# Optimization experiments

Measured on AMD Instinct MI355X. Metric: run time of the kernel, lower is better.

The kernel has to match this reference:

```python
import jax, jax.numpy as jnp
import numpy as np
import math

NUM_GROUPS = 32
NUM_HEADS = 8
EPS = 1e-5

def group_norm(x, w, b):
    B, C, H, W = x.shape
    xg = x.reshape(B, NUM_GROUPS, C // NUM_GROUPS, H, W)
    mu = xg.mean(axis=(2, 3, 4), keepdims=True)
    var = xg.var(axis=(2, 3, 4), keepdims=True)
    xn = ((xg - mu) * jax.lax.rsqrt(var + EPS)).reshape(B, C, H, W)
    return xn * w[None, :, None, None] + b[None, :, None, None]

def layer_norm(t, w, b):
    mu = t.mean(axis=-1, keepdims=True)
    var = t.var(axis=-1, keepdims=True)
    return (t - mu) * jax.lax.rsqrt(var + EPS) * w + b

def setup_inputs() -> dict:
    key = jax.random.key(0)
    ks = jax.random.split(key, 6)
    B, C, H, W, L, D = 32, 512, 32, 32, 77, 768
    return {
        "x": jax.random.normal(ks[0], (B, C, H, W), dtype=jnp.float32),
        "t": jax.random.normal(ks[1], (B, L, D), dtype=jnp.float32),
        "gn_w": jnp.ones((C,), jnp.float32),
        "gn_b": jnp.zeros((C,), jnp.float32),
        "ln_w": jnp.ones((D,), jnp.float32),
        "ln_b": jnp.zeros((D,), jnp.float32),
        "Wq": jax.random.normal(ks[2], (C, C), dtype=jnp.float32) * (1.0 / math.sqrt(C)),
        "Wkv": jax.random.normal(ks[3], (2 * C, D), dtype=jnp.float32) * (1.0 / math.sqrt(D)),
        "Wp": jax.random.normal(ks[4], (C, C), dtype=jnp.float32) * (1.0 / math.sqrt(C)),
        "bp": jnp.zeros((C,), jnp.float32),
    }

def reference(x, t, gn_w, gn_b, ln_w, ln_b, Wq, Wkv, Wp, bp):
    B, C, H, W = x.shape
    L = t.shape[1]
    hd = C // NUM_HEADS
    # q = 1x1 conv (no bias) on GroupNorm(x): [B,C,H,W]
    q = jnp.einsum('bchw,oc->bohw', group_norm(x, gn_w, gn_b), Wq)
    q = q.reshape(B, NUM_HEADS, hd, H * W)            # [B,h,hd,HW]
    # kv = Linear (no bias) on LayerNorm(t): [B,L,2C] -> [B,L,h,2*hd]
    kv = jnp.einsum('bld,od->blo', layer_norm(t, ln_w, ln_b), Wkv)
    kv = kv.reshape(B, L, NUM_HEADS, 2 * hd).transpose(0, 2, 3, 1)  # [B,h,2*hd,L]
    k, v = kv[:, :, :hd, :], kv[:, :, hd:, :]
    scale = 1.0 / math.sqrt(math.sqrt(hd))
    attn = jnp.einsum('bhct,bhcs->bhts', q * scale, k * scale)  # [B,h,HW,L]
    attn = jax.nn.softmax(attn, axis=-1)
    h = jnp.einsum('bhts,bhcs->bhct', attn, v).reshape(B, C, H, W)
    out = jnp.einsum('bchw,oc->bohw', h, Wp) + bp[None, :, None, None]
    return out + x
```

## Files before the change

### kernel.cpp

```cpp
#include <hip/hip_runtime.h>
#include <math.h>

#define NBATCH 32
#define NCH    512
#define NHW    1024
#define NL     77
#define ND     768
#define NHEADS 8

typedef __attribute__((ext_vector_type(8)))  short bf16x8;
typedef __attribute__((ext_vector_type(4)))  float f32x4;
typedef __attribute__((ext_vector_type(4)))  unsigned short ushort4v;
typedef __attribute__((ext_vector_type(8)))  unsigned short ushort8v;

typedef __attribute__((address_space(3))) unsigned int lds_u32;
typedef __attribute__((address_space(1))) const unsigned int glb_u32;

__device__ __forceinline__ void gl_lds16(const void* g, void* l) {
    __builtin_amdgcn_global_load_lds((glb_u32*)g, (lds_u32*)l, 16, 0, 0);
}

__device__ __forceinline__ void split2(float a, unsigned short& h, unsigned short& l) {
    unsigned u  = __float_as_uint(a);
    unsigned rh = (u + 0x7FFFu + ((u >> 16) & 1u)) & 0xFFFF0000u;
    h = (unsigned short)(rh >> 16);
    float res = a - __uint_as_float(rh);
    unsigned v  = __float_as_uint(res);
    unsigned rl = (v + 0x7FFFu + ((v >> 16) & 1u)) & 0xFFFF0000u;
    l = (unsigned short)(rl >> 16);
}

__global__ __launch_bounds__(256) void k_gn_stats(const float* __restrict__ x,
                                                  float* __restrict__ mu_out,
                                                  float* __restrict__ rs_out) {
    const int bg = blockIdx.x;
    const float4* xv = reinterpret_cast<const float4*>(x) + (size_t)bg * 4096;
    float s = 0.f, q = 0.f;
#pragma unroll
    for (int i = 0; i < 16; ++i) {
        float4 v = xv[i * 256 + threadIdx.x];
        s += v.x + v.y + v.z + v.w;
        q += v.x * v.x + v.y * v.y + v.z * v.z + v.w * v.w;
    }
#pragma unroll
    for (int off = 32; off > 0; off >>= 1) {
        s += __shfl_down(s, off);
        q += __shfl_down(q, off);
    }
    __shared__ float rsh[8];
    const int wid = threadIdx.x >> 6;
    if ((threadIdx.x & 63) == 0) { rsh[wid] = s; rsh[4 + wid] = q; }
    __syncthreads();
    if (threadIdx.x == 0) {
        const float S  = rsh[0] + rsh[1] + rsh[2] + rsh[3];
        const float Q  = rsh[4] + rsh[5] + rsh[6] + rsh[7];
        const float mu = S * (1.f / 16384.f);
        const float var = Q * (1.f / 16384.f) - mu * mu;
        mu_out[bg] = mu;
        rs_out[bg] = 1.f / sqrtf(var + 1e-5f);
    }
}

__global__ __launch_bounds__(256) void k_ln(const float* __restrict__ t,
                                            const float* __restrict__ lw,
                                            const float* __restrict__ lb,
                                            float* __restrict__ tln) {
    const int row  = blockIdx.x * 4 + (threadIdx.x >> 6);
    const int lane = threadIdx.x & 63;
    const float4* tv = reinterpret_cast<const float4*>(t + (size_t)row * ND);
    float4 v[3];
    float s = 0.f, q = 0.f;
#pragma unroll
    for (int j = 0; j < 3; ++j) {
        v[j] = tv[lane + j * 64];
        s += v[j].x + v[j].y + v[j].z + v[j].w;
        q += v[j].x * v[j].x + v[j].y * v[j].y + v[j].z * v[j].z + v[j].w * v[j].w;
    }
#pragma unroll
    for (int off = 32; off > 0; off >>= 1) {
        s += __shfl_down(s, off);
        q += __shfl_down(q, off);
    }
    s = __shfl(s, 0);
    q = __shfl(q, 0);
    const float mu  = s * (1.f / 768.f);
    const float rsg = 1.f / sqrtf(q * (1.f / 768.f) - mu * mu + 1e-5f);
    float4* ov = reinterpret_cast<float4*>(tln + (size_t)row * ND);
    const float4* wv = reinterpret_cast<const float4*>(lw);
    const float4* bv = reinterpret_cast<const float4*>(lb);
#pragma unroll
    for (int j = 0; j < 3; ++j) {
        const float4 w = wv[lane + j * 64];
        const float4 bb = bv[lane + j * 64];
        float4 o;
        o.x = (v[j].x - mu) * rsg * w.x + bb.x;
        o.y = (v[j].y - mu) * rsg * w.y + bb.y;
        o.z = (v[j].z - mu) * rsg * w.z + bb.z;
        o.w = (v[j].w - mu) * rsg * w.w + bb.w;
        ov[lane + j * 64] = o;
    }
}

__global__ __launch_bounds__(256) void k_kv(const float* __restrict__ A,
                                            const float* __restrict__ Wkv,
                                            float* __restrict__ kvout) {
    __shared__ float As[16][68];
    __shared__ float Bs[16][132];
    const int n0 = blockIdx.x * 128;
    const int m0 = blockIdx.y * 64;
    const int tid = threadIdx.x;
    const int tm = tid & 15, tn = tid >> 4;
    float acc[4][8];
#pragma unroll
    for (int i = 0; i < 4; ++i)
#pragma unroll
        for (int j = 0; j < 8; ++j) acc[i][j] = 0.f;

    const int arow = tid >> 2, ak4 = (tid & 3) * 4;
    const int brow = tid >> 1, bk8 = (tid & 1) * 8;
    const int arow_g = min(m0 + arow, 2463);
    const float* Aptr = A + (size_t)arow_g * ND;
    const float* Bptr = Wkv + (size_t)(n0 + brow) * ND;

    for (int k0 = 0; k0 < ND; k0 += 16) {
        const float4 av = *reinterpret_cast<const float4*>(Aptr + k0 + ak4);
        const float4 b0 = *reinterpret_cast<const float4*>(Bptr + k0 + bk8);
        const float4 b1 = *reinterpret_cast<const float4*>(Bptr + k0 + bk8 + 4);
        As[ak4 + 0][arow] = av.x; As[ak4 + 1][arow] = av.y;
        As[ak4 + 2][arow] = av.z; As[ak4 + 3][arow] = av.w;
        Bs[bk8 + 0][brow] = b0.x; Bs[bk8 + 1][brow] = b0.y;
        Bs[bk8 + 2][brow] = b0.z; Bs[bk8 + 3][brow] = b0.w;
        Bs[bk8 + 4][brow] = b1.x; Bs[bk8 + 5][brow] = b1.y;
        Bs[bk8 + 6][brow] = b1.z; Bs[bk8 + 7][brow] = b1.w;
        __syncthreads();
#pragma unroll
        for (int k = 0; k < 16; ++k) {
            const float4 a  = *reinterpret_cast<const float4*>(&As[k][tm * 4]);
            const float4 p0 = *reinterpret_cast<const float4*>(&Bs[k][tn * 8]);
            const float4 p1 = *reinterpret_cast<const float4*>(&Bs[k][tn * 8 + 4]);
            const float aa[4] = {a.x, a.y, a.z, a.w};
            const float bb[8] = {p0.x, p0.y, p0.z, p0.w, p1.x, p1.y, p1.z, p1.w};
#pragma unroll
            for (int i = 0; i < 4; ++i)
#pragma unroll
                for (int j = 0; j < 8; ++j)
                    acc[i][j] = fmaf(aa[i], bb[j], acc[i][j]);
        }
        __syncthreads();
    }
#pragma unroll
    for (int i = 0; i < 4; ++i) {
        const int m = m0 + tm * 4 + i;
        if (m < 2464) {
            float* orow = kvout + (size_t)m * 1024 + n0 + tn * 8;
            *reinterpret_cast<float4*>(orow)     = make_float4(acc[i][0], acc[i][1], acc[i][2], acc[i][3]);
            *reinterpret_cast<float4*>(orow + 4) = make_float4(acc[i][4], acc[i][5], acc[i][6], acc[i][7]);
        }
    }
}

__global__ __launch_bounds__(256) void k_wsplit(const float* __restrict__ Wq, const float* __restrict__ Wp,
                                                unsigned short* __restrict__ qh, unsigned short* __restrict__ ql,
                                                unsigned short* __restrict__ ph, unsigned short* __restrict__ pl) {
    const int id = blockIdx.x * 256 + threadIdx.x;
    const bool second = id >= 65536;
    const int e = (second ? id - 65536 : id) * 4;
    const float4 v = *reinterpret_cast<const float4*>((second ? Wp : Wq) + e);
    ushort4v h, l;
    split2(v.x, ((unsigned short*)&h)[0], ((unsigned short*)&l)[0]);
    split2(v.y, ((unsigned short*)&h)[1], ((unsigned short*)&l)[1]);
    split2(v.z, ((unsigned short*)&h)[2], ((unsigned short*)&l)[2]);
    split2(v.w, ((unsigned short*)&h)[3], ((unsigned short*)&l)[3]);
    *reinterpret_cast<ushort4v*>((second ? ph : qh) + e) = h;
    *reinterpret_cast<ushort4v*>((second ? pl : ql) + e) = l;
}

__global__ __launch_bounds__(256) void k_xsplit(const float* __restrict__ x,
                                                const float* __restrict__ mu,
                                                const float* __restrict__ rs,
                                                const float* __restrict__ gw,
                                                const float* __restrict__ gb,
                                                unsigned short* __restrict__ xhi,
                                                unsigned short* __restrict__ xlo) {
    __shared__ float tile[64][68];
    const int b = blockIdx.z, c0 = blockIdx.y * 64, hw0 = blockIdx.x * 64;
    const int tid = threadIdx.x;
    const int ci = tid >> 2, f4 = tid & 3;
    const int c = c0 + ci;
    const float sc = rs[b * 32 + (c >> 4)] * gw[c];
    const float sh = gb[c] - mu[b * 32 + (c >> 4)] * sc;
    const float* src = x + ((size_t)b * NCH + c) * NHW + hw0;
#pragma unroll
    for (int u = 0; u < 4; ++u) {
        float4 v = *reinterpret_cast<const float4*>(src + f4 * 16 + u * 4);
        v.x = v.x * sc + sh; v.y = v.y * sc + sh; v.z = v.z * sc + sh; v.w = v.w * sc + sh;
        *reinterpret_cast<float4*>(&tile[ci][f4 * 16 + u * 4]) = v;
    }
    __syncthreads();
    const int r = tid >> 2, cqi = tid & 3;
    union { ushort8v v[2]; unsigned short s[16]; } H, L;
#pragma unroll
    for (int j = 0; j < 16; ++j)
        split2(tile[cqi * 16 + j][r], H.s[j], L.s[j]);
    const size_t off = ((size_t)b * NHW + hw0 + r) * NCH + c0 + cqi * 16;
    *reinterpret_cast<ushort8v*>(xhi + off)     = H.v[0];
    *reinterpret_cast<ushort8v*>(xhi + off + 8) = H.v[1];
    *reinterpret_cast<ushort8v*>(xlo + off)     = L.v[0];
    *reinterpret_cast<ushort8v*>(xlo + off + 8) = L.v[1];
}

template <int MODE>
__global__ __launch_bounds__(256, 2) void k_projm(const unsigned short* __restrict__ Whi,
                                                  const unsigned short* __restrict__ Wlo,
                                                  const unsigned short* __restrict__ Xhi,
                                                  const unsigned short* __restrict__ Xlo,
                                                  const float* __restrict__ bp,
                                                  const float* __restrict__ xres,
                                                  float* __restrict__ outp) {
    __shared__ char smem[49152];
    const int tid  = threadIdx.x;
    const int lane = tid & 63;
    const int wv   = tid >> 6;
    const int wm   = wv >> 1, wn = wv & 1;
    const int n0 = blockIdx.x * 128;
    const int m0 = blockIdx.y * 256;
    const int b  = blockIdx.z;

    const int xx   = (lane & 7) ^ (lane >> 3);
    const int coff = (xx & 3) * 8;
    const bool lof = xx >= 4;
    const unsigned short* aSrc = (lof ? Wlo : Whi) + (size_t)(m0 + wv * 64 + (lane >> 3)) * NCH + coff;
    const unsigned short* bSrc = (lof ? Xlo : Xhi) + ((size_t)b * NHW + n0 + wv * 32 + (lane >> 3)) * NCH + coff;
    char* aDst = smem + (wv * 64) * 128;
    char* bDst = smem + 32768 + (wv * 32) * 128;

    f32x4 acc[8][4];
#pragma unroll
    for (int i = 0; i < 8; ++i)
#pragma unroll
        for (int j = 0; j < 4; ++j) acc[i][j] = 0.f;

    const char* smA = smem;
    const char* smB = smem + 32768;
    const int swz   = (lane & 7) << 4;
    const int kcol  = (lane >> 4) << 4;
    const int rA0   = wm * 128 + (lane & 15);
    const int rB0   = wn * 64 + (lane & 15);

    for (int k0 = 0; k0 < NCH; k0 += 32) {
#pragma unroll
        for (int j = 0; j < 8; ++j)
            gl_lds16(aSrc + (size_t)j * 8 * NCH, aDst + j * 1024);
#pragma unroll
        for (int j = 0; j < 4; ++j)
            gl_lds16(bSrc + (size_t)j * 8 * NCH, bDst + j * 1024);
        __syncthreads();

        bf16x8 bh[4], bl[4];
#pragma unroll
        for (int ni = 0; ni < 4; ++ni) {
            const int rb = (rB0 + ni * 16) * 128;
            bh[ni] = *reinterpret_cast<const bf16x8*>(smB + rb + (kcol ^ swz));
            bl[ni] = *reinterpret_cast<const bf16x8*>(smB + rb + ((64 + kcol) ^ swz));
        }
#pragma unroll
        for (int mi = 0; mi < 8; ++mi) {
            const int ra = (rA0 + mi * 16) * 128;
            const bf16x8 ah = *reinterpret_cast<const bf16x8*>(smA + ra + (kcol ^ swz));
            const bf16x8 al = *reinterpret_cast<const bf16x8*>(smA + ra + ((64 + kcol) ^ swz));
#pragma unroll
            for (int ni = 0; ni < 4; ++ni) {
                acc[mi][ni] = __builtin_amdgcn_mfma_f32_16x16x32_bf16(ah, bh[ni], acc[mi][ni], 0, 0, 0);
                acc[mi][ni] = __builtin_amdgcn_mfma_f32_16x16x32_bf16(ah, bl[ni], acc[mi][ni], 0, 0, 0);
                acc[mi][ni] = __builtin_amdgcn_mfma_f32_16x16x32_bf16(al, bh[ni], acc[mi][ni], 0, 0, 0);
            }
        }
        __syncthreads();
        aSrc += 32; bSrc += 32;
    }

#pragma unroll
    for (int mi = 0; mi < 8; ++mi) {
#pragma unroll
        for (int ni = 0; ni < 4; ++ni) {
            const int colg = n0 + wn * 64 + ni * 16 + (lane & 15);
#pragma unroll
            for (int reg = 0; reg < 4; ++reg) {
                const int o = m0 + wm * 128 + mi * 16 + ((lane >> 4) << 2) + reg;
                float v = acc[mi][ni][reg];
                const size_t off = ((size_t)b * NCH + o) * NHW + colg;
                if constexpr (MODE == 1) v += bp[o] + xres[off];
                outp[off] = v;
            }
        }
    }
}

__global__ __launch_bounds__(256) void k_attn(const float* __restrict__ q,
                                              const float* __restrict__ kv,
                                              unsigned short* __restrict__ hhi,
                                              unsigned short* __restrict__ hlo) {
    __shared__ float sm[19392];
    float* qs     = sm;
    float* ks     = sm + 4096;
    float* vs     = sm + 9024;
    float* ps     = sm + 13952;
    float* redm   = sm + 18880;
    float* redsum = sm + 19136;
    const int t0  = blockIdx.x * 64;
    const int hh  = blockIdx.y;
    const int b   = blockIdx.z;
    const int tid = threadIdx.x;

    const float* qbase = q + ((size_t)b * NCH + hh * 64) * NHW + t0;
#pragma unroll
    for (int i = 0; i < 4; ++i) {
        const int f4 = i * 256 + tid;
        const int c = f4 >> 4, t4 = (f4 & 15) * 4;
        float4 v = *reinterpret_cast<const float4*>(qbase + (size_t)c * NHW + t4);
        v.x *= 0.125f; v.y *= 0.125f; v.z *= 0.125f; v.w *= 0.125f;
        *reinterpret_cast<float4*>(&qs[c * 64 + t4]) = v;
    }
    const float* kvb = kv + (size_t)b * NL * 1024 + hh * 128;
    for (int f = tid; f < NL * 128; f += 256) {
        const int s = f >> 7, j = f & 127;
        const float val = kvb[(size_t)s * 1024 + j];
        if (j < 64) ks[j * 77 + s] = val;
        else        vs[(j - 64) * 77 + s] = val;
    }
    __syncthreads();

    {
        const int tb = tid & 15, sb = tid >> 4;
        const int s0 = sb * 5;
        float lg[4][5];
#pragma unroll
        for (int i = 0; i < 4; ++i)
#pragma unroll
            for (int j = 0; j < 5; ++j) lg[i][j] = 0.f;
        for (int c = 0; c < 64; ++c) {
            const float4 qv = *reinterpret_cast<const float4*>(&qs[c * 64 + tb * 4]);
            float kk[5];
#pragma unroll
            for (int j = 0; j < 5; ++j) kk[j] = ks[c * 77 + s0 + j];
#pragma unroll
            for (int j = 0; j < 5; ++j) {
                lg[0][j] = fmaf(qv.x, kk[j], lg[0][j]);
                lg[1][j] = fmaf(qv.y, kk[j], lg[1][j]);
                lg[2][j] = fmaf(qv.z, kk[j], lg[2][j]);
                lg[3][j] = fmaf(qv.w, kk[j], lg[3][j]);
            }
        }
#pragma unroll
        for (int j = 0; j < 5; ++j) {
            if (s0 + j < NL) {
#pragma unroll
                for (int i = 0; i < 4; ++i) ps[(s0 + j) * 64 + tb * 4 + i] = lg[i][j];
            }
        }
    }
    __syncthreads();

    {
        const int t = tid & 63, qq = tid >> 6;
        float lmax = -1e30f;
        for (int s = qq; s < NL; s += 4) lmax = fmaxf(lmax, ps[s * 64 + t]);
        redm[qq * 64 + t] = lmax;
        __syncthreads();
        const float gmax = fmaxf(fmaxf(redm[t], redm[64 + t]), fmaxf(redm[128 + t], redm[192 + t]));
        float psum = 0.f;
        for (int s = qq; s < NL; s += 4) psum += __expf(ps[s * 64 + t] - gmax);
        redsum[qq * 64 + t] = psum;
        __syncthreads();
        const float inv = 1.f / (redsum[t] + redsum[64 + t] + redsum[128 + t] + redsum[192 + t]);
        for (int s = qq; s < NL; s += 4) ps[s * 64 + t] = __expf(ps[s * 64 + t] - gmax) * inv;
    }
    __syncthreads();

    {
        const int tb = tid & 15, cb = tid >> 4;
        float acc[4][4];
#pragma unroll
        for (int i = 0; i < 4; ++i)
#pragma unroll
            for (int j = 0; j < 4; ++j) acc[i][j] = 0.f;
        for (int s = 0; s < NL; ++s) {
            const float4 pv = *reinterpret_cast<const float4*>(&ps[s * 64 + tb * 4]);
#pragma unroll
            for (int j = 0; j < 4; ++j) {
                const float vv = vs[(cb * 4 + j) * 77 + s];
                acc[0][j] = fmaf(pv.x, vv, acc[0][j]);
                acc[1][j] = fmaf(pv.y, vv, acc[1][j]);
                acc[2][j] = fmaf(pv.z, vv, acc[2][j]);
                acc[3][j] = fmaf(pv.w, vv, acc[3][j]);
            }
        }
#pragma unroll
        for (int j = 0; j < 4; ++j) {
            *reinterpret_cast<float4*>(&qs[(cb * 4 + j) * 64 + tb * 4]) =
                make_float4(acc[0][j], acc[1][j], acc[2][j], acc[3][j]);
        }
    }
    __syncthreads();
    {
        const int r = tid >> 2, cqi = tid & 3;
        union { ushort8v v[2]; unsigned short s[16]; } H, L;
#pragma unroll
        for (int j = 0; j < 16; ++j)
            split2(qs[(cqi * 16 + j) * 64 + r], H.s[j], L.s[j]);
        const size_t off = ((size_t)b * NHW + t0 + r) * NCH + hh * 64 + cqi * 16;
        *reinterpret_cast<ushort8v*>(hhi + off)     = H.v[0];
        *reinterpret_cast<ushort8v*>(hhi + off + 8) = H.v[1];
        *reinterpret_cast<ushort8v*>(hlo + off)     = L.v[0];
        *reinterpret_cast<ushort8v*>(hlo + off + 8) = L.v[1];
    }
}

extern "C" void kernel_launch(void* const* d_in, const int* in_sizes, int n_in,
                              void* d_out, int out_size, void* d_ws, size_t ws_size,
                              hipStream_t stream) {
    const float* x   = (const float*)d_in[0];
    const float* t   = (const float*)d_in[1];
    const float* gnw = (const float*)d_in[2];
    const float* gnb = (const float*)d_in[3];
    const float* lnw = (const float*)d_in[4];
    const float* lnb = (const float*)d_in[5];
    const float* Wq  = (const float*)d_in[6];
    const float* Wkv = (const float*)d_in[7];
    const float* Wp  = (const float*)d_in[8];
    const float* bp  = (const float*)d_in[9];
    float* out = (float*)d_out;
    float* ws  = (float*)d_ws;

    float* mu  = ws;
    float* rs  = ws + 1024;
    float* tln = ws + 2048;
    float* kvb = ws + 1894400;
    unsigned short* wqh = (unsigned short*)(ws + 2048);
    unsigned short* wql = wqh + 262144;
    unsigned short* wph = wql + 262144;
    unsigned short* wpl = wph + 262144;
    unsigned short* xth = (unsigned short*)(ws + 4417536);
    unsigned short* xtl = xth + 16777216;
    unsigned short* hth = xth;
    unsigned short* htl = xtl;
    float* qb = out;

    k_gn_stats<<<dim3(NBATCH * 32), dim3(256), 0, stream>>>(x, mu, rs);
    k_ln<<<dim3(616), dim3(256), 0, stream>>>(t, lnw, lnb, tln);
    k_kv<<<dim3(8, 39), dim3(256), 0, stream>>>(tln, Wkv, kvb);
    k_wsplit<<<dim3(512), dim3(256), 0, stream>>>(Wq, Wp, wqh, wql, wph, wpl);
    k_xsplit<<<dim3(16, 8, NBATCH), dim3(256), 0, stream>>>(x, mu, rs, gnw, gnb, xth, xtl);
    k_projm<0><<<dim3(8, 2, NBATCH), dim3(256), 0, stream>>>(wqh, wql, xth, xtl,
                                                             nullptr, nullptr, qb);
    k_attn<<<dim3(16, NHEADS, NBATCH), dim3(256), 0, stream>>>(qb, kvb, hth, htl);
    k_projm<1><<<dim3(8, 2, NBATCH), dim3(256), 0, stream>>>(wph, wpl, hth, htl,
                                                             bp, x, out);
}
```

Before: 507.8 us.

## Move attention QK and PV products onto split-bf16 MFMA

The attention kernel's scalar FP32 FMA loops for the Q·K logits and the P·V product become bf16 MFMA ops. Each operand is split into hi/lo bf16 parts, and three MFMAs per tile keep near-FP32 accuracy. Softmax now runs in registers with wave shuffles and no longer subtracts the row max, which removes the LDS reduction passes and several barriers. LDS use grows to about 76 KB with padded layouts, which may reduce occupancy. Skipping the max subtraction also risks overflow in exp if logits are large.

```diff
diff --git a/kernel.cpp b/kernel.cpp
--- a/kernel.cpp
+++ b/kernel.cpp
@@ -296,21 +296,24 @@
     }
 }
 
+#define SP  104
+#define KSP 72
+
 __global__ __launch_bounds__(256) void k_attn(const float* __restrict__ q,
                                               const float* __restrict__ kv,
                                               unsigned short* __restrict__ hhi,
                                               unsigned short* __restrict__ hlo) {
-    __shared__ float sm[19392];
-    float* qs     = sm;
-    float* ks     = sm + 4096;
-    float* vs     = sm + 9024;
-    float* ps     = sm + 13952;
-    float* redm   = sm + 18880;
-    float* redsum = sm + 19136;
-    const int t0  = blockIdx.x * 64;
-    const int hh  = blockIdx.y;
-    const int b   = blockIdx.z;
-    const int tid = threadIdx.x;
+    __shared__ char smem[76288];
+    unsigned short* ks_hi = (unsigned short*)smem;
+    unsigned short* ks_lo = ks_hi + 80 * KSP;
+    unsigned short* vs_hi = (unsigned short*)(smem + 23040);
+    unsigned short* vs_lo = vs_hi + 64 * SP;
+    float*          qst   = (float*)(smem + 49664);
+    unsigned short* p_hi  = (unsigned short*)(smem + 49664);
+    unsigned short* p_lo  = p_hi + 64 * SP;
+
+    const int tid = threadIdx.x, lane = tid & 63, wv = tid >> 6;
+    const int t0 = blockIdx.x * 64, hh = blockIdx.y, b = blockIdx.z;
 
     const float* qbase = q + ((size_t)b * NCH + hh * 64) * NHW + t0;
 #pragma unroll
@@ -319,100 +322,149 @@
         const int c = f4 >> 4, t4 = (f4 & 15) * 4;
         float4 v = *reinterpret_cast<const float4*>(qbase + (size_t)c * NHW + t4);
         v.x *= 0.125f; v.y *= 0.125f; v.z *= 0.125f; v.w *= 0.125f;
-        *reinterpret_cast<float4*>(&qs[c * 64 + t4]) = v;
+        *reinterpret_cast<float4*>(&qst[c * 68 + t4]) = v;
     }
     const float* kvb = kv + (size_t)b * NL * 1024 + hh * 128;
-    for (int f = tid; f < NL * 128; f += 256) {
-        const int s = f >> 7, j = f & 127;
-        const float val = kvb[(size_t)s * 1024 + j];
-        if (j < 64) ks[j * 77 + s] = val;
-        else        vs[(j - 64) * 77 + s] = val;
+#pragma unroll
+    for (int i = 0; i < 10; ++i) {
+        const int f4 = i * 256 + tid;
+        if (f4 < NL * 32) {
+            const int s = f4 >> 5, j4 = (f4 & 31) * 4;
+            const float4 v = *reinterpret_cast<const float4*>(kvb + s * 1024 + j4);
+            unsigned short h0, l0, h1, l1, h2, l2, h3, l3;
+            split2(v.x, h0, l0); split2(v.y, h1, l1);
+            split2(v.z, h2, l2); split2(v.w, h3, l3);
+            if (j4 < 64) {
+                ushort4v H = {h0, h1, h2, h3}, L = {l0, l1, l2, l3};
+                *reinterpret_cast<ushort4v*>(&ks_hi[s * KSP + j4]) = H;
+                *reinterpret_cast<ushort4v*>(&ks_lo[s * KSP + j4]) = L;
+            } else {
+                const int c = j4 - 64;
+                vs_hi[(c + 0) * SP + s] = h0; vs_hi[(c + 1) * SP + s] = h1;
+                vs_hi[(c + 2) * SP + s] = h2; vs_hi[(c + 3) * SP + s] = h3;
+                vs_lo[(c + 0) * SP + s] = l0; vs_lo[(c + 1) * SP + s] = l1;
+                vs_lo[(c + 2) * SP + s] = l2; vs_lo[(c + 3) * SP + s] = l3;
+            }
+        }
+    }
+    for (int z = tid; z < 3 * KSP; z += 256) {
+        const int r = 77 + z / KSP, cc = z % KSP;
+        ks_hi[r * KSP + cc] = 0; ks_lo[r * KSP + cc] = 0;
+    }
+    for (int z = tid; z < 64 * 19; z += 256) {
+        const int c = z / 19, s = 77 + z % 19;
+        vs_hi[c * SP + s] = 0; vs_lo[c * SP + s] = 0;
     }
     __syncthreads();
 
+    bf16x8 qfh[2], qfl[2];
     {
-        const int tb = tid & 15, sb = tid >> 4;
-        const int s0 = sb * 5;
-        float lg[4][5];
-#pragma unroll
-        for (int i = 0; i < 4; ++i)
-#pragma unroll
-            for (int j = 0; j < 5; ++j) lg[i][j] = 0.f;
-        for (int c = 0; c < 64; ++c) {
-            const float4 qv = *reinterpret_cast<const float4*>(&qs[c * 64 + tb * 4]);
-            float kk[5];
-#pragma unroll
-            for (int j = 0; j < 5; ++j) kk[j] = ks[c * 77 + s0 + j];
-#pragma unroll
-            for (int j = 0; j < 5; ++j) {
-                lg[0][j] = fmaf(qv.x, kk[j], lg[0][j]);
-                lg[1][j] = fmaf(qv.y, kk[j], lg[1][j]);
-                lg[2][j] = fmaf(qv.z, kk[j], lg[2][j]);
-                lg[3][j] = fmaf(qv.w, kk[j], lg[3][j]);
-            }
-        }
-#pragma unroll
-        for (int j = 0; j < 5; ++j) {
-            if (s0 + j < NL) {
-#pragma unroll
-                for (int i = 0; i < 4; ++i) ps[(s0 + j) * 64 + tb * 4 + i] = lg[i][j];
-            }
+        const int tq = wv * 16 + (lane & 15);
+#pragma unroll
+        for (int ksx = 0; ksx < 2; ++ksx) {
+            const int cbase = ksx * 32 + (lane >> 4) * 8;
+            union { bf16x8 v; unsigned short u[8]; } H, L;
+#pragma unroll
+            for (int j = 0; j < 8; ++j)
+                split2(qst[(cbase + j) * 68 + tq], H.u[j], L.u[j]);
+            qfh[ksx] = H.v; qfl[ksx] = L.v;
         }
     }
     __syncthreads();
 
-    {
-        const int t = tid & 63, qq = tid >> 6;
-        float lmax = -1e30f;
-        for (int s = qq; s < NL; s += 4) lmax = fmaxf(lmax, ps[s * 64 + t]);
-        redm[qq * 64 + t] = lmax;
-        __syncthreads();
-        const float gmax = fmaxf(fmaxf(redm[t], redm[64 + t]), fmaxf(redm[128 + t], redm[192 + t]));
-        float psum = 0.f;
-        for (int s = qq; s < NL; s += 4) psum += __expf(ps[s * 64 + t] - gmax);
-        redsum[qq * 64 + t] = psum;
-        __syncthreads();
-        const float inv = 1.f / (redsum[t] + redsum[64 + t] + redsum[128 + t] + redsum[192 + t]);
-        for (int s = qq; s < NL; s += 4) ps[s * 64 + t] = __expf(ps[s * 64 + t] - gmax) * inv;
+    for (int z = tid; z < 64 * 16; z += 256) {
+        const int t = z >> 4, s = 80 + (z & 15);
+        p_hi[t * SP + s] = 0; p_lo[t * SP + s] = 0;
+    }
+
+    f32x4 acc[5];
+#pragma unroll
+    for (int sn = 0; sn < 5; ++sn) acc[sn] = 0.f;
+#pragma unroll
+    for (int sn = 0; sn < 5; ++sn) {
+        const int row = sn * 16 + (lane & 15);
+#pragma unroll
+        for (int ksx = 0; ksx < 2; ++ksx) {
+            const int co = ksx * 32 + (lane >> 4) * 8;
+            const bf16x8 kh = *reinterpret_cast<const bf16x8*>(&ks_hi[row * KSP + co]);
+            const bf16x8 kl = *reinterpret_cast<const bf16x8*>(&ks_lo[row * KSP + co]);
+            acc[sn] = __builtin_amdgcn_mfma_f32_16x16x32_bf16(qfh[ksx], kh, acc[sn], 0, 0, 0);
+            acc[sn] = __builtin_amdgcn_mfma_f32_16x16x32_bf16(qfh[ksx], kl, acc[sn], 0, 0, 0);
+            acc[sn] = __builtin_amdgcn_mfma_f32_16x16x32_bf16(qfl[ksx], kh, acc[sn], 0, 0, 0);
+        }
+    }
+
+    const int sl = lane & 15;
+    float pe[5][4];
+    float rowsum[4] = {0.f, 0.f, 0.f, 0.f};
+#pragma unroll
+    for (int sn = 0; sn < 5; ++sn) {
+        const int s = sn * 16 + sl;
+#pragma unroll
+        for (int r = 0; r < 4; ++r) {
+            float p = __expf(acc[sn][r]);
+            p = (s < NL) ? p : 0.f;
+            pe[sn][r] = p;
+            rowsum[r] += p;
+        }
+    }
+#pragma unroll
+    for (int r = 0; r < 4; ++r) {
+#pragma unroll
+        for (int m = 1; m < 16; m <<= 1)
+            rowsum[r] += __shfl_xor(rowsum[r], m);
+    }
+    float inv[4];
+#pragma unroll
+    for (int r = 0; r < 4; ++r) inv[r] = 1.f / rowsum[r];
+
+#pragma unroll
+    for (int sn = 0; sn < 5; ++sn) {
+        const int s = sn * 16 + sl;
+#pragma unroll
+        for (int r = 0; r < 4; ++r) {
+            const int t = wv * 16 + (lane >> 4) * 4 + r;
+            unsigned short ph, pl;
+            split2(pe[sn][r], ph, pl);
+            p_hi[t * SP + s] = ph;
+            p_lo[t * SP + s] = pl;
+        }
     }
     __syncthreads();
 
-    {
-        const int tb = tid & 15, cb = tid >> 4;
-        float acc[4][4];
-#pragma unroll
-        for (int i = 0; i < 4; ++i)
-#pragma unroll
-            for (int j = 0; j < 4; ++j) acc[i][j] = 0.f;
-        for (int s = 0; s < NL; ++s) {
-            const float4 pv = *reinterpret_cast<const float4*>(&ps[s * 64 + tb * 4]);
-#pragma unroll
-            for (int j = 0; j < 4; ++j) {
-                const float vv = vs[(cb * 4 + j) * 77 + s];
-                acc[0][j] = fmaf(pv.x, vv, acc[0][j]);
-                acc[1][j] = fmaf(pv.y, vv, acc[1][j]);
-                acc[2][j] = fmaf(pv.z, vv, acc[2][j]);
-                acc[3][j] = fmaf(pv.w, vv, acc[3][j]);
-            }
-        }
-#pragma unroll
-        for (int j = 0; j < 4; ++j) {
-            *reinterpret_cast<float4*>(&qs[(cb * 4 + j) * 64 + tb * 4]) =
-                make_float4(acc[0][j], acc[1][j], acc[2][j], acc[3][j]);
-        }
-    }
-    __syncthreads();
-    {
-        const int r = tid >> 2, cqi = tid & 3;
-        union { ushort8v v[2]; unsigned short s[16]; } H, L;
-#pragma unroll
-        for (int j = 0; j < 16; ++j)
-            split2(qs[(cqi * 16 + j) * 64 + r], H.s[j], L.s[j]);
-        const size_t off = ((size_t)b * NHW + t0 + r) * NCH + hh * 64 + cqi * 16;
-        *reinterpret_cast<ushort8v*>(hhi + off)     = H.v[0];
-        *reinterpret_cast<ushort8v*>(hhi + off + 8) = H.v[1];
-        *reinterpret_cast<ushort8v*>(hlo + off)     = L.v[0];
-        *reinterpret_cast<ushort8v*>(hlo + off + 8) = L.v[1];
+    f32x4 hacc[4];
+#pragma unroll
+    for (int nt = 0; nt < 4; ++nt) hacc[nt] = 0.f;
+#pragma unroll
+    for (int ksx = 0; ksx < 3; ++ksx) {
+        const int trow = wv * 16 + (lane & 15);
+        const int so = ksx * 32 + (lane >> 4) * 8;
+        const bf16x8 pah = *reinterpret_cast<const bf16x8*>(&p_hi[trow * SP + so]);
+        const bf16x8 pal = *reinterpret_cast<const bf16x8*>(&p_lo[trow * SP + so]);
+#pragma unroll
+        for (int nt = 0; nt < 4; ++nt) {
+            const int crow = nt * 16 + (lane & 15);
+            const bf16x8 vh = *reinterpret_cast<const bf16x8*>(&vs_hi[crow * SP + so]);
+            const bf16x8 vl = *reinterpret_cast<const bf16x8*>(&vs_lo[crow * SP + so]);
+            hacc[nt] = __builtin_amdgcn_mfma_f32_16x16x32_bf16(pah, vh, hacc[nt], 0, 0, 0);
+            hacc[nt] = __builtin_amdgcn_mfma_f32_16x16x32_bf16(pah, vl, hacc[nt], 0, 0, 0);
+            hacc[nt] = __builtin_amdgcn_mfma_f32_16x16x32_bf16(pal, vh, hacc[nt], 0, 0, 0);
+        }
+    }
+
+#pragma unroll
+    for (int nt = 0; nt < 4; ++nt) {
+        const int cg = hh * 64 + nt * 16 + (lane & 15);
+#pragma unroll
+        for (int r = 0; r < 4; ++r) {
+            const int t = t0 + wv * 16 + (lane >> 4) * 4 + r;
+            const float hvf = hacc[nt][r] * inv[r];
+            unsigned short hb, lb;
+            split2(hvf, hb, lb);
+            const size_t off = ((size_t)b * NHW + t) * NCH + cg;
+            hhi[off] = hb;
+            hlo[off] = lb;
+        }
     }
 }
 
```

New measurement: 456.1 us. -10.2%, faster.
